# Performance work log

Hardware: AMD Instinct MI355X
Metric: run time of the kernel (lower is better)

## Reference

```python
import jax, jax.numpy as jnp
import numpy as np


def setup_inputs() -> dict:
    key = jax.random.key(0)
    k1, k2 = jax.random.split(key)
    B, D, H, W = 8, 64, 384, 512
    input1 = jax.random.normal(k1, (B, D, H, W), dtype=jnp.float32)
    input2 = jax.random.normal(k2, (B, 2, H, W), dtype=jnp.float32)  # flow (u, v) in pixels
    return {"input1": input1, "input2": input2}


def reference(input1, input2):
    # Equivalent of: grid = base_grid + 2*flow/(size-1); F.grid_sample(input1, grid,
    # mode='bilinear', padding_mode='border', align_corners=True).
    # With align_corners=True the normalized grid unmaps exactly to pixel coords
    # fx = x + u, fy = y + v; border padding clips coords to the image rectangle.
    B, D, H, W = input1.shape
    dt = input1.dtype
    u = input2[:, 0]  # (B, H, W) horizontal flow
    v = input2[:, 1]  # (B, H, W) vertical flow

    fx = jnp.arange(W, dtype=dt)[None, None, :] + u
    fy = jnp.arange(H, dtype=dt)[None, :, None] + v
    # padding_mode='border': clip sample coordinates to valid range
    fx = jnp.clip(fx, 0.0, W - 1)
    fy = jnp.clip(fy, 0.0, H - 1)

    x0 = jnp.floor(fx)
    y0 = jnp.floor(fy)
    wx = fx - x0  # bilinear weights, (B, H, W)
    wy = fy - y0
    x0i = x0.astype(jnp.int32)
    y0i = y0.astype(jnp.int32)
    x1i = jnp.minimum(x0i + 1, W - 1)
    y1i = jnp.minimum(y0i + 1, H - 1)

    img = jnp.transpose(input1, (0, 2, 3, 1))  # (B, H, W, D) channels-last for gather
    bidx = jnp.arange(B)[:, None, None]

    def gather(yi, xi):
        return img[bidx, yi, xi]  # (B, H, W, D)

    out = (gather(y0i, x0i) * ((1 - wy) * (1 - wx))[..., None]
           + gather(y0i, x1i) * ((1 - wy) * wx)[..., None]
           + gather(y1i, x0i) * (wy * (1 - wx))[..., None]
           + gather(y1i, x1i) * (wy * wx)[..., None])
    return jnp.transpose(out, (0, 3, 1, 2))  # back to (B, D, H, W)
```

## Files before the change

kernel.cpp:

```cpp
#include <hip/hip_runtime.h>

#define Bdim 8
#define Ddim 64
#define Hdim 384
#define Wdim 512

#define TH 4
#define TW 64
#define TILES_W (Wdim / TW)
#define TILES_H (Hdim / TH)
#define TILES_PER_B (TILES_W * TILES_H)


__global__ __launch_bounds__(256, 8) void resample2d_kernel(
    const float* __restrict__ img,
    const float* __restrict__ flow,
    float* __restrict__ out)
{
    const int HW = Hdim * Wdim;

    int bid = blockIdx.x;
    int b   = bid / TILES_PER_B;
    int s   = bid - b * TILES_PER_B;
    int th  = s >> 3;
    int tw  = s & 7;

    int lane = threadIdx.x & 63;
    int wv   = threadIdx.x >> 6;

    int h  = th * TH + wv;
    int w  = tw * TW + lane;
    int hw = h * Wdim + w;

    const float* fb = flow + (size_t)b * 2 * HW;
    float u = __builtin_nontemporal_load(fb + hw);
    float v = __builtin_nontemporal_load(fb + HW + hw);

    float fx = fminf(fmaxf((float)w + u, 0.0f), (float)(Wdim - 1));
    float fy = fminf(fmaxf((float)h + v, 0.0f), (float)(Hdim - 1));

    int x0 = min((int)floorf(fx), Wdim - 2);
    int y0 = min((int)floorf(fy), Hdim - 2);
    float wx = fx - (float)x0;
    float wy = fy - (float)y0;

    float w00 = (1.0f - wy) * (1.0f - wx);
    float w01 = (1.0f - wy) * wx;
    float w10 = wy * (1.0f - wx);
    float w11 = wy * wx;

    int o0 = (y0 * Wdim + x0) * 4;
    int o1 = o0 + Wdim * 4;

    const char* ibc = (const char*)(img + (size_t)b * Ddim * HW);
    float*      ob  = out + (size_t)b * Ddim * HW + hw;

    for (int d0 = 0; d0 < Ddim; d0 += 8) {
        float2 r0[8], r1[8];
        #pragma unroll
        for (int dd = 0; dd < 8; ++dd) {
            const char* p = ibc + (size_t)(d0 + dd) * (HW * 4);
            r0[dd] = *(const float2*)(p + o0);
            r1[dd] = *(const float2*)(p + o1);
        }
        #pragma unroll
        for (int dd = 0; dd < 8; ++dd) {
            float r = r0[dd].x * w00 + r0[dd].y * w01
                    + r1[dd].x * w10 + r1[dd].y * w11;
            __builtin_nontemporal_store(r, ob + (size_t)(d0 + dd) * HW);
        }
    }
}

extern "C" void kernel_launch(void* const* d_in, const int* in_sizes, int n_in,
                              void* d_out, int out_size, void* d_ws, size_t ws_size,
                              hipStream_t stream) {
    const float* img  = (const float*)d_in[0];
    const float* flow = (const float*)d_in[1];
    float* out = (float*)d_out;

    const int total_blocks = Bdim * TILES_PER_B;
    dim3 block(256);
    dim3 grid(total_blocks);
    resample2d_kernel<<<grid, block, 0, stream>>>(img, flow, out);
}
```

Before: 743.3 us.

## Stage haloed image tile in LDS per channel with register-prefetched double buffering

Each block now covers a 16x64 output tile. For every channel it cooperatively loads a 32x96 haloed patch of the input image into shared memory. Bilinear taps are read from LDS when they fall inside the patch and from global memory otherwise. The next channel's patch is prefetched into registers while the current one is computed. The aim is to replace scattered, redundant global gathers with coalesced float4 tile loads, at the cost of four barriers per channel pair, extra halo traffic, and lower occupancy.

```diff
diff --git a/kernel.cpp b/kernel.cpp
--- a/kernel.cpp
+++ b/kernel.cpp
@@ -5,70 +5,130 @@
 #define Hdim 384
 #define Wdim 512
 
-#define TH 4
+#define TH 16
 #define TW 64
 #define TILES_W (Wdim / TW)
 #define TILES_H (Hdim / TH)
 #define TILES_PER_B (TILES_W * TILES_H)
 
+#define YH 32
+#define XW 96
+#define LSTRIDE 104
 
-__global__ __launch_bounds__(256, 8) void resample2d_kernel(
+
+__global__ __launch_bounds__(256, 4) void resample2d_kernel(
     const float* __restrict__ img,
     const float* __restrict__ flow,
     float* __restrict__ out)
 {
+    __shared__ float S[YH * LSTRIDE];
+
     const int HW = Hdim * Wdim;
-
     int bid = blockIdx.x;
     int b   = bid / TILES_PER_B;
     int s   = bid - b * TILES_PER_B;
-    int th  = s >> 3;
-    int tw  = s & 7;
+    int tr  = s >> 3;
+    int tc  = s & 7;
+    int ty  = tr * TH, tx = tc * TW;
 
     int lane = threadIdx.x & 63;
     int wv   = threadIdx.x >> 6;
+    int w    = tx + lane;
 
-    int h  = th * TH + wv;
-    int w  = tw * TW + lane;
-    int hw = h * Wdim + w;
+    int YLO = max(0, min(ty - 8,  Hdim - YH));
+    int XLO = max(0, min(tx - 16, Wdim - XW));
 
     const float* fb = flow + (size_t)b * 2 * HW;
-    float u = __builtin_nontemporal_load(fb + hw);
-    float v = __builtin_nontemporal_load(fb + HW + hw);
+    const float* ib = img  + (size_t)b * Ddim * HW;
+    float*       ob = out  + (size_t)b * Ddim * HW;
 
-    float fx = fminf(fmaxf((float)w + u, 0.0f), (float)(Wdim - 1));
-    float fy = fminf(fmaxf((float)h + v, 0.0f), (float)(Hdim - 1));
+    float w00[4], w01[4], w10[4], w11[4];
+    int   lA[4], gA[4], oA[4];
+    bool  ok[4];
 
-    int x0 = min((int)floorf(fx), Wdim - 2);
-    int y0 = min((int)floorf(fy), Hdim - 2);
-    float wx = fx - (float)x0;
-    float wy = fy - (float)y0;
+    #pragma unroll
+    for (int r = 0; r < 4; ++r) {
+        int h  = ty + wv * 4 + r;
+        int hw = h * Wdim + w;
+        float u = __builtin_nontemporal_load(fb + hw);
+        float v = __builtin_nontemporal_load(fb + HW + hw);
 
-    float w00 = (1.0f - wy) * (1.0f - wx);
-    float w01 = (1.0f - wy) * wx;
-    float w10 = wy * (1.0f - wx);
-    float w11 = wy * wx;
+        float fx = fminf(fmaxf((float)w + u, 0.0f), (float)(Wdim - 1));
+        float fy = fminf(fmaxf((float)h + v, 0.0f), (float)(Hdim - 1));
+        int x0 = min((int)floorf(fx), Wdim - 2);
+        int y0 = min((int)floorf(fy), Hdim - 2);
+        float wx = fx - (float)x0;
+        float wy = fy - (float)y0;
 
-    int o0 = (y0 * Wdim + x0) * 4;
-    int o1 = o0 + Wdim * 4;
+        w00[r] = (1.0f - wy) * (1.0f - wx);
+        w01[r] = (1.0f - wy) * wx;
+        w10[r] = wy * (1.0f - wx);
+        w11[r] = wy * wx;
 
-    const char* ibc = (const char*)(img + (size_t)b * Ddim * HW);
-    float*      ob  = out + (size_t)b * Ddim * HW + hw;
+        gA[r] = y0 * Wdim + x0;
+        lA[r] = (y0 - YLO) * LSTRIDE + (x0 - XLO);
+        oA[r] = hw;
+        ok[r] = (x0 >= XLO) & (x0 <= XLO + XW - 2) &
+                (y0 >= YLO) & (y0 <= YLO + YH - 2);
+    }
 
-    for (int d0 = 0; d0 < Ddim; d0 += 8) {
-        float2 r0[8], r1[8];
+    int goff[3], loff[3];
+    #pragma unroll
+    for (int k = 0; k < 3; ++k) {
+        int i   = (int)threadIdx.x + 256 * k;
+        int row = i / 24;
+        int c   = i - row * 24;
+        goff[k] = (YLO + row) * Wdim + XLO + 4 * c;
+        loff[k] = row * LSTRIDE + 4 * c;
+    }
+
+    auto LOADS = [&](int d, float4& s0, float4& s1, float4& s2) {
+        const float* p = ib + (size_t)d * HW;
+        s0 = *(const float4*)(p + goff[0]);
+        s1 = *(const float4*)(p + goff[1]);
+        s2 = *(const float4*)(p + goff[2]);
+    };
+    auto WRITE = [&](const float4& s0, const float4& s1, const float4& s2) {
+        *(float4*)(&S[loff[0]]) = s0;
+        *(float4*)(&S[loff[1]]) = s1;
+        *(float4*)(&S[loff[2]]) = s2;
+    };
+    auto COMPUTE = [&](int d) {
+        const float* p = ib + (size_t)d * HW;
+        float*       o = ob + (size_t)d * HW;
         #pragma unroll
-        for (int dd = 0; dd < 8; ++dd) {
-            const char* p = ibc + (size_t)(d0 + dd) * (HW * 4);
-            r0[dd] = *(const float2*)(p + o0);
-            r1[dd] = *(const float2*)(p + o1);
+        for (int r = 0; r < 4; ++r) {
+            float f00, f01, f10, f11;
+            if (__builtin_expect((int)ok[r], 1)) {
+                int a = lA[r];
+                f00 = S[a];            f01 = S[a + 1];
+                f10 = S[a + LSTRIDE];  f11 = S[a + LSTRIDE + 1];
+            } else {
+                const float* q = p + gA[r];
+                float2 lo = *(const float2*)q;
+                float2 hi = *(const float2*)(q + Wdim);
+                f00 = lo.x; f01 = lo.y; f10 = hi.x; f11 = hi.y;
+            }
+            float res = f00 * w00[r] + f01 * w01[r]
+                      + f10 * w10[r] + f11 * w11[r];
+            __builtin_nontemporal_store(res, o + oA[r]);
         }
-        #pragma unroll
-        for (int dd = 0; dd < 8; ++dd) {
-            float r = r0[dd].x * w00 + r0[dd].y * w01
-                    + r1[dd].x * w10 + r1[dd].y * w11;
-            __builtin_nontemporal_store(r, ob + (size_t)(d0 + dd) * HW);
-        }
+    };
+
+    float4 a0, a1, a2, b0, b1, b2;
+    LOADS(0, a0, a1, a2);
+    for (int d = 0; d < Ddim; d += 2) {
+        __syncthreads();
+        WRITE(a0, a1, a2);
+        LOADS(d + 1, b0, b1, b2);
+        __syncthreads();
+        COMPUTE(d);
+
+        __syncthreads();
+        WRITE(b0, b1, b2);
+        if (d + 2 < Ddim) LOADS(d + 2, a0, a1, a2);
+        __syncthreads();
+        COMPUTE(d + 1);
     }
 }
 
```

After: 773.5 us. 4.1% more time.
